# Performance work log

Hardware: AMD Instinct MI355X
Metric: run time of the kernel (lower is better)

## Reference

```python
import jax, jax.numpy as jnp
import numpy as np

N_NODES = 50000
N_EDGES = 1_600_000


def gcn_conv(x, W, b, src, dst, ew, n_nodes):
    """PyG GCNConv: out = D^{-1/2}(A+I)D^{-1/2} (x W) + b, deg from edge_weight,
    self-loop weight = 1. Self-loop term handled analytically (norm = dinv[i]^2)."""
    xW = x @ W                                            # [N, F_out]
    deg = jax.ops.segment_sum(ew, dst, num_segments=n_nodes) + 1.0  # +1 self-loop
    dinv = jnp.where(deg > 0, jax.lax.rsqrt(deg), 0.0)    # [N]
    norm = dinv[src] * ew * dinv[dst]                     # [E]
    agg = jax.ops.segment_sum(norm[:, None] * xW[src], dst, num_segments=n_nodes)
    return agg + (dinv * dinv)[:, None] * xW + b


def setup_inputs() -> dict:
    key = jax.random.key(0)
    ks = jax.random.split(key, 9)
    s = lambda fi, fo: 1.0 / np.sqrt(fi)
    return {
        "x": jax.random.normal(ks[0], (N_NODES, 128), dtype=jnp.float32),
        "edge_index": jax.random.randint(ks[1], (2, N_EDGES), 0, N_NODES, dtype=jnp.int64)
        if jax.config.jax_enable_x64 else jax.random.randint(ks[1], (2, N_EDGES), 0, N_NODES, dtype=jnp.int32),
        "edge_weight": jax.random.uniform(ks[2], (N_EDGES,), dtype=jnp.float32),
        "W1": jax.random.normal(ks[3], (128, 64), dtype=jnp.float32) * s(128, 64),
        "b1": jnp.zeros((64,), dtype=jnp.float32),
        "W2": jax.random.normal(ks[4], (64, 64), dtype=jnp.float32) * s(64, 64),
        "b2": jnp.zeros((64,), dtype=jnp.float32),
        "W3": jax.random.normal(ks[5], (64, 40), dtype=jnp.float32) * s(64, 40),
        "b3": jnp.zeros((40,), dtype=jnp.float32),
    }


def reference(x, edge_index, edge_weight, W1, b1, W2, b2, W3, b3):
    src, dst = edge_index[0], edge_index[1]
    n = x.shape[0]
    h = jax.nn.relu(gcn_conv(x, W1, b1, src, dst, edge_weight, n))
    h = jax.nn.relu(gcn_conv(h, W2, b2, src, dst, edge_weight, n))
    return gcn_conv(h, W3, b3, src, dst, edge_weight, n)
```

## Files before the change

kernel.cpp:

```cpp
#include <hip/hip_runtime.h>


#define TILE 4096
#define BCAP_MAX 9216

static __device__ __forceinline__ float4 f4zero() { return make_float4(0.f, 0.f, 0.f, 0.f); }

static __device__ __forceinline__ unsigned short f2bf_rne(float x) {
    unsigned u = __float_as_uint(x);
    u += 0x7FFFu + ((u >> 16) & 1u);
    return (unsigned short)(u >> 16);
}
static __device__ __forceinline__ float bf2f(unsigned short b) {
    return __uint_as_float((unsigned)b << 16);
}

__global__ __launch_bounds__(1024) void bin_count_kernel(
        const int* __restrict__ dst, int* __restrict__ cnt, int E, int ntiles) {
    __shared__ int h[256];
    const int tid = threadIdx.x;
    const int t = blockIdx.x;
    if (tid < 256) h[tid] = 0;
    __syncthreads();
    const int e0 = t * TILE;
    #pragma unroll
    for (int j = 0; j < 4; ++j) {
        int e = e0 + j * 1024 + tid;
        if (e < E) atomicAdd(&h[dst[e] >> 8], 1);
    }
    __syncthreads();
    if (tid < 256) cnt[tid * ntiles + t] = h[tid];
}

__global__ __launch_bounds__(512) void bin_scan_kernel(
        int* __restrict__ cnt, int* __restrict__ bintotal, int ntiles) {
    __shared__ int buf[512];
    const int b = blockIdx.x;
    const int tid = threadIdx.x;
    int v = (tid < ntiles) ? cnt[b * ntiles + tid] : 0;
    buf[tid] = v;
    __syncthreads();
    for (int off = 1; off < 512; off <<= 1) {
        int x = buf[tid];
        int a = (tid >= off) ? buf[tid - off] : 0;
        __syncthreads();
        buf[tid] = x + a;
        __syncthreads();
    }
    if (tid < ntiles) cnt[b * ntiles + tid] = buf[tid] - v;
    if (tid == 0) bintotal[b] = buf[511];
}

__global__ __launch_bounds__(1024) void bin_scatter_kernel(
        const int* __restrict__ src, const int* __restrict__ dst,
        const float* __restrict__ ew, const int* __restrict__ cntbase,
        int2* __restrict__ binned, int E, int bcap, int ntiles) {
    __shared__ int cnt[256];
    __shared__ int scan[256];
    __shared__ int gbase[256];
    __shared__ int2 sorted[TILE];
    __shared__ unsigned char binof[TILE];
    const int tid = threadIdx.x;
    const int t = blockIdx.x;
    const int e0 = t * TILE;

    if (tid < 256) cnt[tid] = 0;
    __syncthreads();

    int mypk[4]; float myew[4]; int mybin[4]; int myrank[4]; bool myok[4];
    #pragma unroll
    for (int j = 0; j < 4; ++j) {
        int e = e0 + j * 1024 + tid;
        myok[j] = (e < E);
        if (myok[j]) {
            int d = dst[e];
            int s = src[e];
            myew[j]   = ew[e];
            mybin[j]  = d >> 8;
            mypk[j]   = (s << 8) | (d & 255);
            myrank[j] = atomicAdd(&cnt[mybin[j]], 1);
        }
    }
    __syncthreads();
    if (tid < 256) scan[tid] = cnt[tid];
    __syncthreads();
    for (int off = 1; off < 256; off <<= 1) {
        int v = 0;
        if (tid < 256) { v = scan[tid]; if (tid >= off) v += scan[tid - off]; }
        __syncthreads();
        if (tid < 256) scan[tid] = v;
        __syncthreads();
    }
    if (tid < 256) gbase[tid] = cntbase[tid * ntiles + t];
    __syncthreads();
    #pragma unroll
    for (int j = 0; j < 4; ++j) {
        if (myok[j]) {
            int b = mybin[j];
            int slot = (scan[b] - cnt[b]) + myrank[j];
            sorted[slot] = make_int2(mypk[j], __float_as_int(myew[j]));
            binof[slot]  = (unsigned char)b;
        }
    }
    __syncthreads();
    const int total = scan[255];
    for (int i = tid; i < total; i += 1024) {
        int b = binof[i];
        int pos = gbase[b] + (i - (scan[b] - cnt[b]));
        if (pos < bcap)
            binned[(size_t)b * bcap + pos] = sorted[i];
    }
}

__global__ __launch_bounds__(1024) void bin_group_kernel(
        int2* __restrict__ binned, const int* __restrict__ bintotal,
        int* __restrict__ row_start, int* __restrict__ row_cnt,
        float* __restrict__ dinv, int N, int bcap) {
    __shared__ int   cntl[256];
    __shared__ float degl[256];
    __shared__ int   scan[256];
    __shared__ int   run[256];
    __shared__ int2  sorted[BCAP_MAX];
    const int b = blockIdx.x;
    const int tid = threadIdx.x;
    int n = bintotal[b];
    if (n > bcap) n = bcap;
    if (tid < 256) { cntl[tid] = 0; degl[tid] = 0.f; }
    __syncthreads();

    int2* seg = binned + (size_t)b * bcap;
    for (int i = tid; i < n; i += 1024) {
        int2 v = seg[i];
        int dl = v.x & 255;
        atomicAdd(&cntl[dl], 1);
        atomicAdd(&degl[dl], __int_as_float(v.y));
    }
    __syncthreads();
    if (tid < 256) scan[tid] = cntl[tid];
    __syncthreads();
    for (int off = 1; off < 256; off <<= 1) {
        int v = 0;
        if (tid < 256) { v = scan[tid]; if (tid >= off) v += scan[tid - off]; }
        __syncthreads();
        if (tid < 256) scan[tid] = v;
        __syncthreads();
    }
    if (tid < 256) {
        int ex = scan[tid] - cntl[tid];
        int d = (b << 8) + tid;
        if (d < N) {
            row_start[d] = b * bcap + ex;
            row_cnt[d]   = cntl[tid];
            dinv[d]      = rsqrtf(degl[tid] + 1.0f);
        }
        run[tid] = ex;
    }
    __syncthreads();
    for (int i = tid; i < n; i += 1024) {
        int2 v = seg[i];
        int dl = v.x & 255;
        int r = atomicAdd(&run[dl], 1);
        sorted[r] = make_int2(v.x >> 8, v.y);
    }
    __syncthreads();
    for (int i = tid; i < n; i += 1024)
        seg[i] = sorted[i];
}

template <int K, int M>
__global__ __launch_bounds__(256) void gemm_kernel(const float* __restrict__ X,
        const float* __restrict__ W, const float* __restrict__ dinv,
        unsigned short* __restrict__ Y, int N) {
    constexpr int KP = K + 4;
    __shared__ float xs[64 * KP];
    __shared__ float ws[K * M];
    const int tid = threadIdx.x;
    const int row0 = blockIdx.x * 64;

    for (int i = tid * 4; i < K * M; i += 1024)
        *(float4*)&ws[i] = *(const float4*)&W[i];

    const int nrows = min(64, N - row0);
    for (int i = tid * 4; i < 64 * K; i += 1024) {
        int r = i / K, k = i % K;
        float4 v = f4zero();
        if (r < nrows) v = *(const float4*)&X[(size_t)(row0 + r) * K + k];
        *(float4*)&xs[r * KP + k] = v;
    }
    __syncthreads();

    const int ct = tid & 15, rt = tid >> 4;
    const bool cok = (ct * 4 < M);
    float acc[4][4] = {};
    for (int k = 0; k < K; ++k) {
        float a0 = xs[(rt +  0) * KP + k];
        float a1 = xs[(rt + 16) * KP + k];
        float a2 = xs[(rt + 32) * KP + k];
        float a3 = xs[(rt + 48) * KP + k];
        float4 bv = cok ? *(const float4*)&ws[k * M + ct * 4] : f4zero();
        acc[0][0] += a0 * bv.x; acc[0][1] += a0 * bv.y; acc[0][2] += a0 * bv.z; acc[0][3] += a0 * bv.w;
        acc[1][0] += a1 * bv.x; acc[1][1] += a1 * bv.y; acc[1][2] += a1 * bv.z; acc[1][3] += a1 * bv.w;
        acc[2][0] += a2 * bv.x; acc[2][1] += a2 * bv.y; acc[2][2] += a2 * bv.z; acc[2][3] += a2 * bv.w;
        acc[3][0] += a3 * bv.x; acc[3][1] += a3 * bv.y; acc[3][2] += a3 * bv.z; acc[3][3] += a3 * bv.w;
    }
    if (cok) {
        #pragma unroll
        for (int i = 0; i < 4; ++i) {
            int r = row0 + rt + 16 * i;
            if (r < N) {
                float dd = dinv[r];
                ushort4 o;
                o.x = f2bf_rne(acc[i][0] * dd); o.y = f2bf_rne(acc[i][1] * dd);
                o.z = f2bf_rne(acc[i][2] * dd); o.w = f2bf_rne(acc[i][3] * dd);
                *(ushort4*)&Y[(size_t)r * M + ct * 4] = o;
            }
        }
    }
}

template <int F, bool RELU>
__global__ __launch_bounds__(256) void agg_kernel(const unsigned short* __restrict__ xw,
        const int2* __restrict__ csr, const int* __restrict__ row_start,
        const int* __restrict__ row_cnt, const float* __restrict__ dinv,
        const float* __restrict__ bias, float* __restrict__ out, int N) {
    int wid = (int)((blockIdx.x * blockDim.x + threadIdx.x) >> 6);
    int lane = threadIdx.x & 63;
    if (wid >= N) return;
    const int2* row = csr + row_start[wid];
    int cnt = row_cnt[wid];
    float acc0 = 0.f, acc1 = 0.f;
    for (int base = 0; base < cnt; base += 64) {
        int m = min(cnt - base, 64);
        int2 ed = make_int2(0, 0);
        if (lane < m) ed = row[base + lane];
        int j = 0;
        for (; j + 8 <= m; j += 8) {
            #pragma unroll
            for (int u = 0; u < 8; u += 2) {
                int s0 = __builtin_amdgcn_readlane(ed.x, j + u);
                int w0 = __builtin_amdgcn_readlane(ed.y, j + u);
                int s1 = __builtin_amdgcn_readlane(ed.x, j + u + 1);
                int w1 = __builtin_amdgcn_readlane(ed.y, j + u + 1);
                acc0 = fmaf(__int_as_float(w0), bf2f(xw[(size_t)s0 * F + lane]), acc0);
                acc1 = fmaf(__int_as_float(w1), bf2f(xw[(size_t)s1 * F + lane]), acc1);
            }
        }
        for (; j < m; ++j) {
            int s = __builtin_amdgcn_readlane(ed.x, j);
            int w = __builtin_amdgcn_readlane(ed.y, j);
            acc0 = fmaf(__int_as_float(w), bf2f(xw[(size_t)s * F + lane]), acc0);
        }
    }
    if (lane < F) {
        float dd = dinv[wid];
        float selfv = bf2f(xw[(size_t)wid * F + lane]);
        float acc = dd * (acc0 + acc1 + selfv) + bias[lane];
        if (RELU) acc = fmaxf(acc, 0.f);
        out[(size_t)wid * F + lane] = acc;
    }
}

static inline size_t ws_align(size_t x) { return (x + 255) & ~(size_t)255; }

extern "C" void kernel_launch(void* const* d_in, const int* in_sizes, int n_in,
                              void* d_out, int out_size, void* d_ws, size_t ws_size,
                              hipStream_t stream) {
    const float* x  = (const float*)d_in[0];
    const int*   ei = (const int*)d_in[1];
    const float* ew = (const float*)d_in[2];
    const float* W1 = (const float*)d_in[3];
    const float* b1 = (const float*)d_in[4];
    const float* W2 = (const float*)d_in[5];
    const float* b2 = (const float*)d_in[6];
    const float* W3 = (const float*)d_in[7];
    const float* b3 = (const float*)d_in[8];
    float* out = (float*)d_out;

    const int N = in_sizes[0] / 128;
    const int E = in_sizes[1] / 2;
    const int* src = ei;
    const int* dst = ei + E;
    const int nbins = (N + 255) >> 8;
    const int ntiles = (E + TILE - 1) / TILE;

    char* p = (char*)d_ws;
    size_t off = 0;
    auto alloc = [&](size_t bytes) -> char* {
        char* q = p + off;
        off = ws_align(off + bytes);
        return q;
    };
    int*   row_start = (int*)  alloc((size_t)N * 4);
    int*   row_cnt   = (int*)  alloc((size_t)N * 4);
    float* dinv      = (float*)alloc((size_t)N * 4);
    int*   cntbase   = (int*)  alloc((size_t)256 * ntiles * 4);
    int*   bintotal  = (int*)  alloc((size_t)256 * 4);
    unsigned short* xwbuf = (unsigned short*)alloc((size_t)N * 64 * 2);
    float* hbuf      = (float*)alloc((size_t)N * 64 * 4);
    size_t remain = (ws_size > off) ? (ws_size - off) : 0;
    int bcap = (int)(remain / ((size_t)nbins * 8));
    if (bcap > BCAP_MAX) bcap = BCAP_MAX;
    int2* binned = (int2*)alloc((size_t)nbins * (size_t)bcap * 8);

    const int gb = (N + 63) / 64;
    const int ab = (N + 3) / 4;

    bin_count_kernel<<<ntiles, 1024, 0, stream>>>(dst, cntbase, E, ntiles);
    bin_scan_kernel<<<256, 512, 0, stream>>>(cntbase, bintotal, ntiles);
    bin_scatter_kernel<<<ntiles, 1024, 0, stream>>>(src, dst, ew, cntbase, binned, E, bcap, ntiles);
    bin_group_kernel<<<nbins, 1024, 0, stream>>>(binned, bintotal, row_start, row_cnt, dinv, N, bcap);

    gemm_kernel<128, 64><<<gb, 256, 0, stream>>>(x, W1, dinv, xwbuf, N);
    agg_kernel<64, true><<<ab, 256, 0, stream>>>(xwbuf, binned, row_start, row_cnt, dinv, b1, hbuf, N);
    gemm_kernel<64, 64><<<gb, 256, 0, stream>>>(hbuf, W2, dinv, xwbuf, N);
    agg_kernel<64, true><<<ab, 256, 0, stream>>>(xwbuf, binned, row_start, row_cnt, dinv, b2, hbuf, N);
    gemm_kernel<64, 40><<<gb, 256, 0, stream>>>(hbuf, W3, dinv, xwbuf, N);
    agg_kernel<40, false><<<ab, 256, 0, stream>>>(xwbuf, binned, row_start, row_cnt, dinv, b3, out, N);
}
```

Before: 289.0 us.

## Split bf16 feature matrix into column planes and aggregate each plane separately

The GEMM now writes its bf16 output as two column planes: the first 32 columns, then the rest. Aggregation runs twice per layer, once per plane, and each wavefront handles two edges at a time (half-wave per edge) before combining the halves with a cross-half shuffle. The aim is a smaller gathered working set per pass, 64 B rows, so it fits better in cache and gathers get more locality. The cost is reading the CSR edge list twice per layer, doubling the aggregation launches, and idle lanes in the 8-wide last plane.

```diff
diff --git a/kernel.cpp b/kernel.cpp
--- a/kernel.cpp
+++ b/kernel.cpp
@@ -190,14 +190,15 @@
     __syncthreads();
 
     const int ct = tid & 15, rt = tid >> 4;
-    const bool cok = (ct * 4 < M);
+    const int c = ct * 4;
+    const bool cok = (c < M);
     float acc[4][4] = {};
     for (int k = 0; k < K; ++k) {
         float a0 = xs[(rt +  0) * KP + k];
         float a1 = xs[(rt + 16) * KP + k];
         float a2 = xs[(rt + 32) * KP + k];
         float a3 = xs[(rt + 48) * KP + k];
-        float4 bv = cok ? *(const float4*)&ws[k * M + ct * 4] : f4zero();
+        float4 bv = cok ? *(const float4*)&ws[k * M + c] : f4zero();
         acc[0][0] += a0 * bv.x; acc[0][1] += a0 * bv.y; acc[0][2] += a0 * bv.z; acc[0][3] += a0 * bv.w;
         acc[1][0] += a1 * bv.x; acc[1][1] += a1 * bv.y; acc[1][2] += a1 * bv.z; acc[1][3] += a1 * bv.w;
         acc[2][0] += a2 * bv.x; acc[2][1] += a2 * bv.y; acc[2][2] += a2 * bv.z; acc[2][3] += a2 * bv.w;
@@ -212,14 +213,18 @@
                 ushort4 o;
                 o.x = f2bf_rne(acc[i][0] * dd); o.y = f2bf_rne(acc[i][1] * dd);
                 o.z = f2bf_rne(acc[i][2] * dd); o.w = f2bf_rne(acc[i][3] * dd);
-                *(ushort4*)&Y[(size_t)r * M + ct * 4] = o;
+                unsigned short* dp;
+                if (c < 32) dp = &Y[(size_t)r * 32 + c];
+                else        dp = &Y[(size_t)N * 32 + (size_t)r * (M - 32) + (c - 32)];
+                *(ushort4*)dp = o;
             }
         }
     }
 }
 
-template <int F, bool RELU>
-__global__ __launch_bounds__(256) void agg_kernel(const unsigned short* __restrict__ xw,
+template <int FH, int FTOT, int COFF, bool RELU>
+__global__ __launch_bounds__(256) void agg_half_kernel(
+        const unsigned short* __restrict__ xwh,
         const int2* __restrict__ csr, const int* __restrict__ row_start,
         const int* __restrict__ row_cnt, const float* __restrict__ dinv,
         const float* __restrict__ bias, float* __restrict__ out, int N) {
@@ -228,7 +233,10 @@
     if (wid >= N) return;
     const int2* row = csr + row_start[wid];
     int cnt = row_cnt[wid];
-    float acc0 = 0.f, acc1 = 0.f;
+    const int col = lane & 31;
+    const int hi  = lane >> 5;
+    const bool cok = (col < FH);
+    float acc = 0.f;
     for (int base = 0; base < cnt; base += 64) {
         int m = min(cnt - base, 64);
         int2 ed = make_int2(0, 0);
@@ -236,27 +244,35 @@
         int j = 0;
         for (; j + 8 <= m; j += 8) {
             #pragma unroll
-            for (int u = 0; u < 8; u += 2) {
-                int s0 = __builtin_amdgcn_readlane(ed.x, j + u);
-                int w0 = __builtin_amdgcn_readlane(ed.y, j + u);
-                int s1 = __builtin_amdgcn_readlane(ed.x, j + u + 1);
-                int w1 = __builtin_amdgcn_readlane(ed.y, j + u + 1);
-                acc0 = fmaf(__int_as_float(w0), bf2f(xw[(size_t)s0 * F + lane]), acc0);
-                acc1 = fmaf(__int_as_float(w1), bf2f(xw[(size_t)s1 * F + lane]), acc1);
+            for (int p = 0; p < 8; p += 2) {
+                int sA = __builtin_amdgcn_readlane(ed.x, j + p);
+                int wA = __builtin_amdgcn_readlane(ed.y, j + p);
+                int sB = __builtin_amdgcn_readlane(ed.x, j + p + 1);
+                int wB = __builtin_amdgcn_readlane(ed.y, j + p + 1);
+                int s   = hi ? sB : sA;
+                float w = __int_as_float(hi ? wB : wA);
+                if (cok) acc = fmaf(w, bf2f(xwh[(size_t)s * FH + col]), acc);
             }
         }
-        for (; j < m; ++j) {
-            int s = __builtin_amdgcn_readlane(ed.x, j);
-            int w = __builtin_amdgcn_readlane(ed.y, j);
-            acc0 = fmaf(__int_as_float(w), bf2f(xw[(size_t)s * F + lane]), acc0);
-        }
-    }
-    if (lane < F) {
+        for (; j < m; j += 2) {
+            int sA = __builtin_amdgcn_readlane(ed.x, j);
+            int wA = __builtin_amdgcn_readlane(ed.y, j);
+            int s = sA; float w = __int_as_float(wA);
+            if (j + 1 < m) {
+                int sB = __builtin_amdgcn_readlane(ed.x, j + 1);
+                int wB = __builtin_amdgcn_readlane(ed.y, j + 1);
+                if (hi) { s = sB; w = __int_as_float(wB); }
+            } else if (hi) { w = 0.f; }
+            if (cok) acc = fmaf(w, bf2f(xwh[(size_t)s * FH + col]), acc);
+        }
+    }
+    acc += __shfl_xor(acc, 32);
+    if (lane < FH) {
         float dd = dinv[wid];
-        float selfv = bf2f(xw[(size_t)wid * F + lane]);
-        float acc = dd * (acc0 + acc1 + selfv) + bias[lane];
-        if (RELU) acc = fmaxf(acc, 0.f);
-        out[(size_t)wid * F + lane] = acc;
+        float selfv = bf2f(xwh[(size_t)wid * FH + lane]);
+        float v = dd * (acc + selfv) + bias[COFF + lane];
+        if (RELU) v = fmaxf(v, 0.f);
+        out[(size_t)wid * FTOT + COFF + lane] = v;
     }
 }
 
@@ -302,6 +318,8 @@
     if (bcap > BCAP_MAX) bcap = BCAP_MAX;
     int2* binned = (int2*)alloc((size_t)nbins * (size_t)bcap * 8);
 
+    const unsigned short* plane1 = xwbuf + (size_t)N * 32;
+
     const int gb = (N + 63) / 64;
     const int ab = (N + 3) / 4;
 
@@ -311,9 +329,12 @@
     bin_group_kernel<<<nbins, 1024, 0, stream>>>(binned, bintotal, row_start, row_cnt, dinv, N, bcap);
 
     gemm_kernel<128, 64><<<gb, 256, 0, stream>>>(x, W1, dinv, xwbuf, N);
-    agg_kernel<64, true><<<ab, 256, 0, stream>>>(xwbuf, binned, row_start, row_cnt, dinv, b1, hbuf, N);
+    agg_half_kernel<32, 64,  0, true ><<<ab, 256, 0, stream>>>(xwbuf,  binned, row_start, row_cnt, dinv, b1, hbuf, N);
+    agg_half_kernel<32, 64, 32, true ><<<ab, 256, 0, stream>>>(plane1, binned, row_start, row_cnt, dinv, b1, hbuf, N);
     gemm_kernel<64, 64><<<gb, 256, 0, stream>>>(hbuf, W2, dinv, xwbuf, N);
-    agg_kernel<64, true><<<ab, 256, 0, stream>>>(xwbuf, binned, row_start, row_cnt, dinv, b2, hbuf, N);
+    agg_half_kernel<32, 64,  0, true ><<<ab, 256, 0, stream>>>(xwbuf,  binned, row_start, row_cnt, dinv, b2, hbuf, N);
+    agg_half_kernel<32, 64, 32, true ><<<ab, 256, 0, stream>>>(plane1, binned, row_start, row_cnt, dinv, b2, hbuf, N);
     gemm_kernel<64, 40><<<gb, 256, 0, stream>>>(hbuf, W3, dinv, xwbuf, N);
-    agg_kernel<40, false><<<ab, 256, 0, stream>>>(xwbuf, binned, row_start, row_cnt, dinv, b3, out, N);
-}
+    agg_half_kernel<32, 40,  0, false><<<ab, 256, 0, stream>>>(xwbuf,  binned, row_start, row_cnt, dinv, b3, out, N);
+    agg_half_kernel< 8, 40, 32, false><<<ab, 256, 0, stream>>>(plane1, binned, row_start, row_cnt, dinv, b3, out, N);
+}
```

After: 382.9 us. +32.5%, slower.

## Load CSR edges via scalar s_load and store pre-scaled byte offsets

Applied to the files above, without the earlier changes.

The aggregation kernel now fetches edge (src, weight) pairs through wave-uniform scalar loads (two s_load_dwordx16 per 16 edges) instead of a vector load followed by readlane. Source indices are pre-shifted into byte offsets at group time. The xW buffer now uses a fixed 64-wide row stride so one offset works for every layer. This is meant to drop vector memory and readlane traffic from the edge stream and to simplify address arithmetic. In exchange, the tail block over-reads past each row, which is why 512 bytes of workspace are reserved, and each 16-edge block waits on lgkmcnt(0) with no prefetch overlap.

```diff
diff --git a/kernel.cpp b/kernel.cpp
--- a/kernel.cpp
+++ b/kernel.cpp
@@ -3,6 +3,8 @@
 
 #define TILE 4096
 #define BCAP_MAX 9216
+
+typedef int s16i __attribute__((ext_vector_type(16)));
 
 static __device__ __forceinline__ float4 f4zero() { return make_float4(0.f, 0.f, 0.f, 0.f); }
 
@@ -160,7 +162,7 @@
         int2 v = seg[i];
         int dl = v.x & 255;
         int r = atomicAdd(&run[dl], 1);
-        sorted[r] = make_int2(v.x >> 8, v.y);
+        sorted[r] = make_int2((v.x >> 8) << 7, v.y);
     }
     __syncthreads();
     for (int i = tid; i < n; i += 1024)
@@ -190,14 +192,15 @@
     __syncthreads();
 
     const int ct = tid & 15, rt = tid >> 4;
-    const bool cok = (ct * 4 < M);
+    const int c = ct * 4;
+    const bool cok = (c < M);
     float acc[4][4] = {};
     for (int k = 0; k < K; ++k) {
         float a0 = xs[(rt +  0) * KP + k];
         float a1 = xs[(rt + 16) * KP + k];
         float a2 = xs[(rt + 32) * KP + k];
         float a3 = xs[(rt + 48) * KP + k];
-        float4 bv = cok ? *(const float4*)&ws[k * M + ct * 4] : f4zero();
+        float4 bv = cok ? *(const float4*)&ws[k * M + c] : f4zero();
         acc[0][0] += a0 * bv.x; acc[0][1] += a0 * bv.y; acc[0][2] += a0 * bv.z; acc[0][3] += a0 * bv.w;
         acc[1][0] += a1 * bv.x; acc[1][1] += a1 * bv.y; acc[1][2] += a1 * bv.z; acc[1][3] += a1 * bv.w;
         acc[2][0] += a2 * bv.x; acc[2][1] += a2 * bv.y; acc[2][2] += a2 * bv.z; acc[2][3] += a2 * bv.w;
@@ -212,51 +215,84 @@
                 ushort4 o;
                 o.x = f2bf_rne(acc[i][0] * dd); o.y = f2bf_rne(acc[i][1] * dd);
                 o.z = f2bf_rne(acc[i][2] * dd); o.w = f2bf_rne(acc[i][3] * dd);
-                *(ushort4*)&Y[(size_t)r * M + ct * 4] = o;
+                *(ushort4*)&Y[(size_t)r * 64 + c] = o;
             }
         }
     }
 }
 
-template <int F, bool RELU>
-__global__ __launch_bounds__(256) void agg_kernel(const unsigned short* __restrict__ xw,
+template <int FOUT, bool RELU>
+__global__ __launch_bounds__(256) void agg_kernel(
+        const unsigned short* __restrict__ xw,
         const int2* __restrict__ csr, const int* __restrict__ row_start,
         const int* __restrict__ row_cnt, const float* __restrict__ dinv,
         const float* __restrict__ bias, float* __restrict__ out, int N) {
     int wid = (int)((blockIdx.x * blockDim.x + threadIdx.x) >> 6);
     int lane = threadIdx.x & 63;
     if (wid >= N) return;
-    const int2* row = csr + row_start[wid];
-    int cnt = row_cnt[wid];
+
+    const unsigned rs  = (unsigned)__builtin_amdgcn_readfirstlane(row_start[wid]);
+    const int      cnt = __builtin_amdgcn_readfirstlane(row_cnt[wid]);
+    unsigned long long addr = (unsigned long long)csr + (unsigned long long)rs * 8ull;
+    const char* xwb = (const char*)xw;
+
     float acc0 = 0.f, acc1 = 0.f;
-    for (int base = 0; base < cnt; base += 64) {
-        int m = min(cnt - base, 64);
-        int2 ed = make_int2(0, 0);
-        if (lane < m) ed = row[base + lane];
-        int j = 0;
-        for (; j + 8 <= m; j += 8) {
-            #pragma unroll
-            for (int u = 0; u < 8; u += 2) {
-                int s0 = __builtin_amdgcn_readlane(ed.x, j + u);
-                int w0 = __builtin_amdgcn_readlane(ed.y, j + u);
-                int s1 = __builtin_amdgcn_readlane(ed.x, j + u + 1);
-                int w1 = __builtin_amdgcn_readlane(ed.y, j + u + 1);
-                acc0 = fmaf(__int_as_float(w0), bf2f(xw[(size_t)s0 * F + lane]), acc0);
-                acc1 = fmaf(__int_as_float(w1), bf2f(xw[(size_t)s1 * F + lane]), acc1);
+    int j = 0;
+    for (; j + 16 <= cnt; j += 16) {
+        s16i edA, edB;
+        asm volatile("s_load_dwordx16 %0, %2, 0x0\n\t"
+                     "s_load_dwordx16 %1, %2, 0x40\n\t"
+                     "s_waitcnt lgkmcnt(0)"
+                     : "=&s"(edA), "=&s"(edB) : "s"(addr));
+        #pragma unroll
+        for (int p = 0; p < 8; ++p) {
+            const unsigned short* pp = (const unsigned short*)(xwb + (unsigned)edA[2 * p]);
+            float xv = bf2f(pp[lane]);
+            float w  = __int_as_float(edA[2 * p + 1]);
+            if (p & 1) acc1 = fmaf(w, xv, acc1); else acc0 = fmaf(w, xv, acc0);
+        }
+        #pragma unroll
+        for (int p = 0; p < 8; ++p) {
+            const unsigned short* pp = (const unsigned short*)(xwb + (unsigned)edB[2 * p]);
+            float xv = bf2f(pp[lane]);
+            float w  = __int_as_float(edB[2 * p + 1]);
+            if (p & 1) acc1 = fmaf(w, xv, acc1); else acc0 = fmaf(w, xv, acc0);
+        }
+        addr += 128ull;
+    }
+    if (j < cnt) {
+        const int r = cnt - j;
+        s16i edA, edB;
+        asm volatile("s_load_dwordx16 %0, %2, 0x0\n\t"
+                     "s_load_dwordx16 %1, %2, 0x40\n\t"
+                     "s_waitcnt lgkmcnt(0)"
+                     : "=&s"(edA), "=&s"(edB) : "s"(addr));
+        #pragma unroll
+        for (int p = 0; p < 8; ++p) {
+            if (p < r) {
+                const unsigned short* pp = (const unsigned short*)(xwb + (unsigned)edA[2 * p]);
+                float xv = bf2f(pp[lane]);
+                float w  = __int_as_float(edA[2 * p + 1]);
+                if (p & 1) acc1 = fmaf(w, xv, acc1); else acc0 = fmaf(w, xv, acc0);
             }
         }
-        for (; j < m; ++j) {
-            int s = __builtin_amdgcn_readlane(ed.x, j);
-            int w = __builtin_amdgcn_readlane(ed.y, j);
-            acc0 = fmaf(__int_as_float(w), bf2f(xw[(size_t)s * F + lane]), acc0);
-        }
-    }
-    if (lane < F) {
+        #pragma unroll
+        for (int p = 0; p < 8; ++p) {
+            if (p + 8 < r) {
+                const unsigned short* pp = (const unsigned short*)(xwb + (unsigned)edB[2 * p]);
+                float xv = bf2f(pp[lane]);
+                float w  = __int_as_float(edB[2 * p + 1]);
+                if (p & 1) acc1 = fmaf(w, xv, acc1); else acc0 = fmaf(w, xv, acc0);
+            }
+        }
+    }
+
+    if (lane < FOUT) {
         float dd = dinv[wid];
-        float selfv = bf2f(xw[(size_t)wid * F + lane]);
-        float acc = dd * (acc0 + acc1 + selfv) + bias[lane];
-        if (RELU) acc = fmaxf(acc, 0.f);
-        out[(size_t)wid * F + lane] = acc;
+        float selfv = bf2f(xw[(size_t)wid * 64 + lane]);
+        float v = dd * (acc0 + acc1 + selfv) + bias[lane];
+        if (RELU) v = fmaxf(v, 0.f);
+        out[(size_t)wid * FOUT + lane] = v;
     }
 }
 
@@ -297,7 +333,7 @@
     int*   bintotal  = (int*)  alloc((size_t)256 * 4);
     unsigned short* xwbuf = (unsigned short*)alloc((size_t)N * 64 * 2);
     float* hbuf      = (float*)alloc((size_t)N * 64 * 4);
-    size_t remain = (ws_size > off) ? (ws_size - off) : 0;
+    size_t remain = (ws_size > off + 512) ? (ws_size - off - 512) : 0;
     int bcap = (int)(remain / ((size_t)nbins * 8));
     if (bcap > BCAP_MAX) bcap = BCAP_MAX;
     int2* binned = (int2*)alloc((size_t)nbins * (size_t)bcap * 8);
@@ -311,9 +347,9 @@
     bin_group_kernel<<<nbins, 1024, 0, stream>>>(binned, bintotal, row_start, row_cnt, dinv, N, bcap);
 
     gemm_kernel<128, 64><<<gb, 256, 0, stream>>>(x, W1, dinv, xwbuf, N);
-    agg_kernel<64, true><<<ab, 256, 0, stream>>>(xwbuf, binned, row_start, row_cnt, dinv, b1, hbuf, N);
+    agg_kernel<64, true ><<<ab, 256, 0, stream>>>(xwbuf, binned, row_start, row_cnt, dinv, b1, hbuf, N);
     gemm_kernel<64, 64><<<gb, 256, 0, stream>>>(hbuf, W2, dinv, xwbuf, N);
-    agg_kernel<64, true><<<ab, 256, 0, stream>>>(xwbuf, binned, row_start, row_cnt, dinv, b2, hbuf, N);
+    agg_kernel<64, true ><<<ab, 256, 0, stream>>>(xwbuf, binned, row_start, row_cnt, dinv, b2, hbuf, N);
     gemm_kernel<64, 40><<<gb, 256, 0, stream>>>(hbuf, W3, dinv, xwbuf, N);
     agg_kernel<40, false><<<ab, 256, 0, stream>>>(xwbuf, binned, row_start, row_cnt, dinv, b3, out, N);
 }
```

After: 293.4 us. No clear change (+1.5%).

## Vectorize aggregation gathers: 8 edges per wave with 16-byte bf16 row loads

Applied to the files above, without the earlier changes.

The aggregation kernel now splits each wave into 8 groups of 8 lanes. Each group handles one edge and loads a full 128-byte bf16 row as uint4 per lane, replacing the per-edge scalar 2-byte loads. Edge metadata is broadcast with ds_bpermute, the next 64-edge chunk is prefetched, and partial sums are combined with xor shuffles. CSR source indices are pre-scaled to byte offsets and the xw buffer is padded to a 64-wide stride so the 40-wide layer can use the same path. In exchange it adds a shuffle reduction and extra reads of padding columns.

```diff
diff --git a/kernel.cpp b/kernel.cpp
--- a/kernel.cpp
+++ b/kernel.cpp
@@ -11,9 +11,8 @@
     u += 0x7FFFu + ((u >> 16) & 1u);
     return (unsigned short)(u >> 16);
 }
-static __device__ __forceinline__ float bf2f(unsigned short b) {
-    return __uint_as_float((unsigned)b << 16);
-}
+static __device__ __forceinline__ float bflo(unsigned u) { return __uint_as_float(u << 16); }
+static __device__ __forceinline__ float bfhi(unsigned u) { return __uint_as_float(u & 0xffff0000u); }
 
 __global__ __launch_bounds__(1024) void bin_count_kernel(
         const int* __restrict__ dst, int* __restrict__ cnt, int E, int ntiles) {
@@ -160,7 +159,7 @@
         int2 v = seg[i];
         int dl = v.x & 255;
         int r = atomicAdd(&run[dl], 1);
-        sorted[r] = make_int2(v.x >> 8, v.y);
+        sorted[r] = make_int2((v.x >> 8) << 7, v.y);
     }
     __syncthreads();
     for (int i = tid; i < n; i += 1024)
@@ -190,14 +189,15 @@
     __syncthreads();
 
     const int ct = tid & 15, rt = tid >> 4;
-    const bool cok = (ct * 4 < M);
+    const int c = ct * 4;
+    const bool cok = (c < M);
     float acc[4][4] = {};
     for (int k = 0; k < K; ++k) {
         float a0 = xs[(rt +  0) * KP + k];
         float a1 = xs[(rt + 16) * KP + k];
         float a2 = xs[(rt + 32) * KP + k];
         float a3 = xs[(rt + 48) * KP + k];
-        float4 bv = cok ? *(const float4*)&ws[k * M + ct * 4] : f4zero();
+        float4 bv = cok ? *(const float4*)&ws[k * M + c] : f4zero();
         acc[0][0] += a0 * bv.x; acc[0][1] += a0 * bv.y; acc[0][2] += a0 * bv.z; acc[0][3] += a0 * bv.w;
         acc[1][0] += a1 * bv.x; acc[1][1] += a1 * bv.y; acc[1][2] += a1 * bv.z; acc[1][3] += a1 * bv.w;
         acc[2][0] += a2 * bv.x; acc[2][1] += a2 * bv.y; acc[2][2] += a2 * bv.z; acc[2][3] += a2 * bv.w;
@@ -212,51 +212,90 @@
                 ushort4 o;
                 o.x = f2bf_rne(acc[i][0] * dd); o.y = f2bf_rne(acc[i][1] * dd);
                 o.z = f2bf_rne(acc[i][2] * dd); o.w = f2bf_rne(acc[i][3] * dd);
-                *(ushort4*)&Y[(size_t)r * M + ct * 4] = o;
+                *(ushort4*)&Y[(size_t)r * 64 + c] = o;
             }
         }
     }
 }
 
-template <int F, bool RELU>
-__global__ __launch_bounds__(256) void agg_kernel(const unsigned short* __restrict__ xw,
+template <int FOUT, bool RELU>
+__global__ __launch_bounds__(256) void agg_kernel(
+        const unsigned short* __restrict__ xw,
         const int2* __restrict__ csr, const int* __restrict__ row_start,
         const int* __restrict__ row_cnt, const float* __restrict__ dinv,
         const float* __restrict__ bias, float* __restrict__ out, int N) {
     int wid = (int)((blockIdx.x * blockDim.x + threadIdx.x) >> 6);
     int lane = threadIdx.x & 63;
     if (wid >= N) return;
+
     const int2* row = csr + row_start[wid];
-    int cnt = row_cnt[wid];
-    float acc0 = 0.f, acc1 = 0.f;
+    const int   cnt = row_cnt[wid];
+    const char* xwb = (const char*)xw;
+
+    const int g = lane >> 3;
+    const unsigned li16 = (unsigned)(lane & 7) * 16u;
+    const int g4 = g << 2;
+
+    float acc[8] = {0.f, 0.f, 0.f, 0.f, 0.f, 0.f, 0.f, 0.f};
+
+    int2 edA = make_int2(0, 0);
+    if (lane < cnt) edA = row[lane];
+
     for (int base = 0; base < cnt; base += 64) {
-        int m = min(cnt - base, 64);
-        int2 ed = make_int2(0, 0);
-        if (lane < m) ed = row[base + lane];
-        int j = 0;
-        for (; j + 8 <= m; j += 8) {
-            #pragma unroll
-            for (int u = 0; u < 8; u += 2) {
-                int s0 = __builtin_amdgcn_readlane(ed.x, j + u);
-                int w0 = __builtin_amdgcn_readlane(ed.y, j + u);
-                int s1 = __builtin_amdgcn_readlane(ed.x, j + u + 1);
-                int w1 = __builtin_amdgcn_readlane(ed.y, j + u + 1);
-                acc0 = fmaf(__int_as_float(w0), bf2f(xw[(size_t)s0 * F + lane]), acc0);
-                acc1 = fmaf(__int_as_float(w1), bf2f(xw[(size_t)s1 * F + lane]), acc1);
-            }
-        }
-        for (; j < m; ++j) {
-            int s = __builtin_amdgcn_readlane(ed.x, j);
-            int w = __builtin_amdgcn_readlane(ed.y, j);
-            acc0 = fmaf(__int_as_float(w), bf2f(xw[(size_t)s * F + lane]), acc0);
-        }
-    }
-    if (lane < F) {
+        const int m = min(cnt - base, 64);
+        int2 edN = make_int2(0, 0);
+        const int nb = base + 64;
+        if (nb < cnt) {
+            if (lane < cnt - nb) edN = row[nb + lane];
+        }
+        int bidx = g4;
+        #pragma unroll 2
+        for (int t = 0; t * 8 < m; ++t, bidx += 32) {
+            unsigned off = (unsigned)__builtin_amdgcn_ds_bpermute(bidx, edA.x);
+            unsigned wu  = (unsigned)__builtin_amdgcn_ds_bpermute(bidx, edA.y);
+            const bool valid = (t * 8 + g) < m;
+            off = valid ? off : 0u;
+            float wf = valid ? __uint_as_float(wu) : 0.f;
+            uint4 rv = *(const uint4*)(xwb + (size_t)(off + li16));
+            acc[0] = fmaf(wf, bflo(rv.x), acc[0]);
+            acc[1] = fmaf(wf, bfhi(rv.x), acc[1]);
+            acc[2] = fmaf(wf, bflo(rv.y), acc[2]);
+            acc[3] = fmaf(wf, bfhi(rv.y), acc[3]);
+            acc[4] = fmaf(wf, bflo(rv.z), acc[4]);
+            acc[5] = fmaf(wf, bfhi(rv.z), acc[5]);
+            acc[6] = fmaf(wf, bflo(rv.w), acc[6]);
+            acc[7] = fmaf(wf, bfhi(rv.w), acc[7]);
+        }
+        edA = edN;
+    }
+
+    #pragma unroll
+    for (int o = 8; o <= 32; o <<= 1) {
+        #pragma unroll
+        for (int t = 0; t < 8; ++t)
+            acc[t] += __shfl_xor(acc[t], o);
+    }
+
+    if (lane < FOUT / 8) {
+        const int f0 = lane * 8;
+        uint4 sr = *(const uint4*)(xwb + ((unsigned)wid * 128u + li16));
         float dd = dinv[wid];
-        float selfv = bf2f(xw[(size_t)wid * F + lane]);
-        float acc = dd * (acc0 + acc1 + selfv) + bias[lane];
-        if (RELU) acc = fmaxf(acc, 0.f);
-        out[(size_t)wid * F + lane] = acc;
+        float4 bv0 = *(const float4*)&bias[f0];
+        float4 bv1 = *(const float4*)&bias[f0 + 4];
+        float r0 = dd * (acc[0] + bflo(sr.x)) + bv0.x;
+        float r1 = dd * (acc[1] + bfhi(sr.x)) + bv0.y;
+        float r2 = dd * (acc[2] + bflo(sr.y)) + bv0.z;
+        float r3 = dd * (acc[3] + bfhi(sr.y)) + bv0.w;
+        float r4 = dd * (acc[4] + bflo(sr.z)) + bv1.x;
+        float r5 = dd * (acc[5] + bfhi(sr.z)) + bv1.y;
+        float r6 = dd * (acc[6] + bflo(sr.w)) + bv1.z;
+        float r7 = dd * (acc[7] + bfhi(sr.w)) + bv1.w;
+        if (RELU) {
+            r0 = fmaxf(r0, 0.f); r1 = fmaxf(r1, 0.f); r2 = fmaxf(r2, 0.f); r3 = fmaxf(r3, 0.f);
+            r4 = fmaxf(r4, 0.f); r5 = fmaxf(r5, 0.f); r6 = fmaxf(r6, 0.f); r7 = fmaxf(r7, 0.f);
+        }
+        *(float4*)&out[(size_t)wid * FOUT + f0]     = make_float4(r0, r1, r2, r3);
+        *(float4*)&out[(size_t)wid * FOUT + f0 + 4] = make_float4(r4, r5, r6, r7);
     }
 }
 
@@ -297,7 +336,7 @@
     int*   bintotal  = (int*)  alloc((size_t)256 * 4);
     unsigned short* xwbuf = (unsigned short*)alloc((size_t)N * 64 * 2);
     float* hbuf      = (float*)alloc((size_t)N * 64 * 4);
-    size_t remain = (ws_size > off) ? (ws_size - off) : 0;
+    size_t remain = (ws_size > off + 512) ? (ws_size - off - 512) : 0;
     int bcap = (int)(remain / ((size_t)nbins * 8));
     if (bcap > BCAP_MAX) bcap = BCAP_MAX;
     int2* binned = (int2*)alloc((size_t)nbins * (size_t)bcap * 8);
@@ -311,9 +350,9 @@
     bin_group_kernel<<<nbins, 1024, 0, stream>>>(binned, bintotal, row_start, row_cnt, dinv, N, bcap);
 
     gemm_kernel<128, 64><<<gb, 256, 0, stream>>>(x, W1, dinv, xwbuf, N);
-    agg_kernel<64, true><<<ab, 256, 0, stream>>>(xwbuf, binned, row_start, row_cnt, dinv, b1, hbuf, N);
+    agg_kernel<64, true ><<<ab, 256, 0, stream>>>(xwbuf, binned, row_start, row_cnt, dinv, b1, hbuf, N);
     gemm_kernel<64, 64><<<gb, 256, 0, stream>>>(hbuf, W2, dinv, xwbuf, N);
-    agg_kernel<64, true><<<ab, 256, 0, stream>>>(xwbuf, binned, row_start, row_cnt, dinv, b2, hbuf, N);
+    agg_kernel<64, true ><<<ab, 256, 0, stream>>>(xwbuf, binned, row_start, row_cnt, dinv, b2, hbuf, N);
     gemm_kernel<64, 40><<<gb, 256, 0, stream>>>(hbuf, W3, dinv, xwbuf, N);
     agg_kernel<40, false><<<ab, 256, 0, stream>>>(xwbuf, binned, row_start, row_cnt, dinv, b3, out, N);
 }
```

Measured after the change: 269.3 us. 6.8% less time.
